# Kernel tuning notes

Measured on AMD Instinct MI355X. Metric: run time of the kernel, lower is better.

Reference implementation:

```python
import jax, jax.numpy as jnp
import numpy as np

S = 2048   # sample_batch
N = 16     # num_h (agents per sample group)
OBS = 8
PRED = 12
H = 16     # hidden / embed size


def _lstm_cell(x, h, c, Wi, Wh, b):
    # torch LSTMCell gate order: i, f, g, o
    g = x @ Wi + h @ Wh + b
    i, f, gg, o = jnp.split(g, 4, axis=-1)
    c = jax.nn.sigmoid(f) * c + jax.nn.sigmoid(i) * jnp.tanh(gg)
    h = jax.nn.sigmoid(o) * jnp.tanh(c)
    return h, c


def setup_inputs() -> dict:
    key = jax.random.key(0)
    ks = jax.random.split(key, 16)
    B = S * N
    p = lambda k, sh: jax.random.normal(k, sh, jnp.float32) * 0.1
    return dict(
        traj_rel=jax.random.normal(ks[0], (OBS, B, 2), jnp.float32),
        obs_traj_pos=jax.random.normal(ks[1], (OBS, B, 2), jnp.float32),
        nei_index=jax.random.randint(ks[2], (B, N), 0, 2, jnp.int32),
        noise=jax.random.normal(ks[3], (PRED, B, 2), jnp.float32),
        enc_emb_W=p(ks[4], (2, H)), enc_emb_b=jnp.zeros((H,), jnp.float32),
        enc_Wi=p(ks[5], (H, 4 * H)), enc_Wh=p(ks[6], (H, 4 * H)), enc_b=jnp.zeros((4 * H,), jnp.float32),
        dec_in_W=p(ks[7], (H + 2, H)), dec_in_b=jnp.zeros((H,), jnp.float32),
        dec_Wi=p(ks[8], (H, 4 * H)), dec_Wh=p(ks[9], (H, 4 * H)), dec_b=jnp.zeros((4 * H,), jnp.float32),
        pool_rel_W=p(ks[10], (2, H)), pool_rel_b=jnp.zeros((H,), jnp.float32),
        pool_mlp_W=p(ks[11], (2 * H, H)), pool_mlp_b=jnp.zeros((H,), jnp.float32),
        out_W=p(ks[12], (H, 4)), out_b=jnp.zeros((4,), jnp.float32),
    )


def reference(traj_rel, obs_traj_pos, nei_index, noise,
              enc_emb_W, enc_emb_b, enc_Wi, enc_Wh, enc_b,
              dec_in_W, dec_in_b, dec_Wi, dec_Wh, dec_b,
              pool_rel_W, pool_rel_b, pool_mlp_W, pool_mlp_b,
              out_W, out_b):
    B = traj_rel.shape[1]
    mask = nei_index > 0  # (B, N)

    # --- history encoder: embed + LSTM over obs steps, take last hidden ---
    def enc_step(carry, x):
        h, c = carry
        e = jax.nn.relu(x @ enc_emb_W + enc_emb_b)
        h, c = _lstm_cell(e, h, c, enc_Wi, enc_Wh, enc_b)
        return (h, c), None

    h0 = jnp.zeros((B, H), traj_rel.dtype)
    (h_enc, _), _ = jax.lax.scan(enc_step, (h0, h0), traj_rel[:OBS])

    # --- neighbor pooling: embed relative pos, concat neighbor hidden, MLP, masked max-pool ---
    def pool(rel, h):
        re = jax.nn.relu(rel @ pool_rel_W + pool_rel_b)  # (B, N, H)
        hn = jnp.broadcast_to(h.reshape(S, 1, N, H), (S, N, N, H)).reshape(B, N, H)
        feat = jax.nn.relu(jnp.concatenate([re, hn], -1) @ pool_mlp_W + pool_mlp_b)
        masked = jnp.where(mask[..., None], feat, -1e9)
        pooled = masked.max(axis=1)  # (B, H)
        has = mask.any(axis=1, keepdims=True)
        return jnp.where(has, pooled, 0.0)

    def dec_step(carry, noise_t):
        h, c, ctx, out, pos = carry
        inp = jax.lax.stop_gradient(jnp.concatenate([ctx, out], -1))  # .detach() in torch
        e = jax.nn.relu(inp @ dec_in_W + dec_in_b)
        h, c = _lstm_cell(e, h, c, dec_Wi, dec_Wh, dec_b)
        p = pos.reshape(S, N, 2)
        # rel[s,i,j] = pos[s,i] - pos[s,j]  (matches expand/transpose subtraction)
        rel = (p[:, :, None, :] - p[:, None, :, :]).reshape(B, N, 2)
        ctx = pool(rel, h)
        o4 = (h + ctx) @ out_W + out_b
        mu = o4[:, :2]
        scale = jnp.clip(o4[:, 2:], -9.0, 4.0)
        std = jnp.exp(scale)
        pred = mu + std * noise_t
        pos = jax.lax.stop_gradient(pos + pred)
        return (h, c, ctx, pred, pos), (pred, mu, std)

    init = (h_enc, jnp.zeros_like(h_enc), jnp.zeros_like(h_enc),
            traj_rel[OBS - 1], obs_traj_pos[-1])
    _, (pred, mu, std) = jax.lax.scan(dec_step, init, noise)
    return pred, mu, std  # each (PRED, B, 2)
```

## Files before the change

kernel.cpp:

```cpp
#include <hip/hip_runtime.h>

#define S_    2048
#define N_    16
#define OBS_  8
#define PRED_ 12
#define B_    (S_*N_)

typedef __attribute__((ext_vector_type(8))) short short8;
typedef __attribute__((ext_vector_type(4))) float floatx4;
typedef __attribute__((ext_vector_type(4))) unsigned uintx4;
typedef unsigned short ushort_t;

__device__ __forceinline__ float sigmf(float x) { return __builtin_amdgcn_rcpf(1.0f + __expf(-x)); }
__device__ __forceinline__ float tanhx(float x) { return fmaf(-2.0f, __builtin_amdgcn_rcpf(1.0f + __expf(2.0f*x)), 1.0f); }
__device__ __forceinline__ unsigned bfhi(float f) {
  return __builtin_bit_cast(unsigned, f) + 0x8000u;
}
__device__ __forceinline__ unsigned pack2bf(float lo, float hi) {
  return __builtin_amdgcn_perm(bfhi(hi), bfhi(lo), 0x07060302);
}
__device__ __forceinline__ ushort_t f2bf1(float f) { return (ushort_t)(bfhi(f) >> 16); }

extern "C" __global__ __launch_bounds__(256, 4) void traj_ar_kernel(
    const float* __restrict__ traj_rel, const float* __restrict__ obs_pos,
    const int*  __restrict__ nei,       const float* __restrict__ noise,
    const float* __restrict__ eeW, const float* __restrict__ eeb,
    const float* __restrict__ eWi, const float* __restrict__ eWh, const float* __restrict__ eb,
    const float* __restrict__ diW, const float* __restrict__ dib,
    const float* __restrict__ dWi, const float* __restrict__ dWh, const float* __restrict__ db,
    const float* __restrict__ prW, const float* __restrict__ prb,
    const float* __restrict__ mW,  const float* __restrict__ mb,
    const float* __restrict__ oW,  const float* __restrict__ ob,
    float* __restrict__ out)
{
  __shared__ __align__(16) float sW_pr[32];
  __shared__ __align__(16) float sb_pr[16];
  __shared__ __align__(16) float sW_o[64];
  __shared__ __align__(16) float sb_o[4];
  __shared__ __align__(16) float h_s[256];
  __shared__ __align__(16) float ctx_s[256];
  __shared__ __align__(16) float g_s[4*256];
  __shared__ __align__(16) ushort_t e_bf[16*24];
  __shared__ __align__(16) ushort_t hb_s[16*24];
  __shared__ __align__(16) ushort_t ctx_bf[16*24];
  __shared__ __align__(16) ushort_t re_s[16*392];
  __shared__ __align__(16) float pos_s[32];
  __shared__ __align__(16) float prev_s[32];
  __shared__ __align__(16) ushort_t prev_bf[32];
  __shared__            unsigned sm_s[16];

  const int tid = threadIdx.x;
  const int s = blockIdx.x;
  const int i = tid >> 4;
  const int k = tid & 15;
  const int bi = s*N_ + i;
  const int lq = (tid & 63) >> 4;
  const int lc = tid & 15;
  const int w  = tid >> 6;

  if (tid < 32) sW_pr[tid] = prW[tid];
  if (tid < 16) sb_pr[tid] = prb[tid];
  if (tid < 64) sW_o[tid] = oW[tid];
  if (tid < 4)  sb_o[tid] = ob[tid];
  if (tid < 192) ((unsigned*)hb_s)[tid] = 0;
  if (tid < 192) ((unsigned*)ctx_bf)[tid] = 0;

  if (k < 2) {
    float pv = traj_rel[((OBS_-1)*B_ + bi)*2 + k];
    prev_s[i*2+k] = pv;
    prev_bf[i*2+k] = f2bf1(pv);
    pos_s[i*2+k]  = obs_pos[((OBS_-1)*B_ + bi)*2 + k];
  }

  short8 bfrag;
  {
    uintx4 bw;
    #pragma unroll
    for (int p = 0; p < 4; ++p)
      bw[p] = pack2bf(mW[(8*lq + 2*p)*16 + lc], mW[(8*lq + 2*p + 1)*16 + lc]);
    bfrag = __builtin_bit_cast(short8, bw);
  }
  const float bm = mb[lc];

  const float w0k = eeW[k], w1k = eeW[16+k], bek = eeb[k];

  short8 gA; floatx4 gC;
  {
    const int row0 = (lq & 1) * 8;
    const float* gsrc = (lq & 2) ? eWh : eWi;
    uintx4 aw;
    #pragma unroll
    for (int p = 0; p < 4; ++p)
      aw[p] = pack2bf(gsrc[(row0+2*p)*64 + w*16 + lc], gsrc[(row0+2*p+1)*64 + w*16 + lc]);
    gA = __builtin_bit_cast(short8, aw);
    #pragma unroll
    for (int r = 0; r < 4; ++r) gC[r] = eb[w*16 + lq*4 + r];
  }

  unsigned long long bal = __ballot(nei[bi*N_ + k] > 0);
  if (k == 0) sm_s[i] = (unsigned)((bal >> (16*(i & 3))) & 0xFFFFull);

  __syncthreads();

  float c_reg = 0.0f;
  const float2* xr2 = (const float2*)traj_rel;
  for (int t = 0; t < OBS_; ++t) {
    {
      float2 x = xr2[t*B_ + bi];
      float e = fmaxf(fmaf(x.y, w1k, fmaf(x.x, w0k, bek)), 0.0f);
      e_bf[i*24 + k] = f2bf1(e);
    }
    __syncthreads();
    {
      const ushort_t* bp = (lq < 2) ? &e_bf[lc*24 + (lq&1)*8] : &hb_s[lc*24 + (lq&1)*8];
      short8 bfr = *(const short8*)bp;
      floatx4 d = __builtin_amdgcn_mfma_f32_16x16x32_bf16(gA, bfr, gC, 0, 0, 0);
      *(floatx4*)&g_s[w*256 + lc*16 + lq*4] = d;
    }
    __syncthreads();
    {
      float gI = g_s[0*256 + i*16 + k];
      float gF = g_s[1*256 + i*16 + k];
      float gG = g_s[2*256 + i*16 + k];
      float gO = g_s[3*256 + i*16 + k];
      float ig = sigmf(gI), fg = sigmf(gF), gv = tanhx(gG), og = sigmf(gO);
      c_reg = fg*c_reg + ig*gv;
      float nh = og * tanhx(c_reg);
      hb_s[i*24 + k] = f2bf1(nh);
    }
  }

  short8 dA; floatx4 dC;
  {
    const int row0 = (lq & 1) * 8;
    const float* gsrc = (lq & 2) ? dWh : dWi;
    uintx4 aw;
    #pragma unroll
    for (int p = 0; p < 4; ++p)
      aw[p] = pack2bf(gsrc[(row0+2*p)*64 + w*16 + lc], gsrc[(row0+2*p+1)*64 + w*16 + lc]);
    dA = __builtin_bit_cast(short8, aw);
    #pragma unroll
    for (int r = 0; r < 4; ++r) dC[r] = db[w*16 + lq*4 + r];
  }

  short8 diA; floatx4 diC;
  {
    uintx4 aw; aw[0]=0; aw[1]=0; aw[2]=0; aw[3]=0;
    if (lq < 2) {
      const int r0 = lq*8;
      #pragma unroll
      for (int p = 0; p < 4; ++p)
        aw[p] = pack2bf(diW[(r0+2*p)*16 + lc], diW[(r0+2*p+1)*16 + lc]);
    } else if (lq == 2) {
      aw[0] = pack2bf(diW[16*16 + lc], diW[17*16 + lc]);
    }
    diA = __builtin_bit_cast(short8, aw);
    #pragma unroll
    for (int r = 0; r < 4; ++r) diC[r] = dib[lq*4 + r];
  }

  floatx4 cm0, cm1, cm2, cm3;
  {
    #pragma unroll
    for (int tt = 0; tt < 4; ++tt) {
      const unsigned mi = sm_s[4*w + tt];
      floatx4 cf;
      #pragma unroll
      for (int r = 0; r < 4; ++r)
        cf[r] = ((mi >> (lq*4 + r)) & 1u) ? bm : -1e9f;
      if (tt==0) cm0=cf; else if (tt==1) cm1=cf; else if (tt==2) cm2=cf; else cm3=cf;
    }
  }

  c_reg = 0.0f;
  const int MU_OFF = PRED_*B_*2;
  const int SD_OFF = 2*PRED_*B_*2;
  for (int t = 0; t < PRED_; ++t) {
    const float nz = noise[(t*B_ + bi)*2 + (k & 1)];
    {
      short8 cv = *(const short8*)&ctx_bf[lc*24 + (lq&1)*8];
      uintx4 pz; pz[0] = *(const unsigned*)&prev_bf[lc*2]; pz[1]=0; pz[2]=0; pz[3]=0;
      short8 pv = __builtin_bit_cast(short8, pz);
      short8 zz = {0,0,0,0,0,0,0,0};
      short8 bfr = (lq < 2) ? cv : ((lq == 2) ? pv : zz);
      floatx4 d = __builtin_amdgcn_mfma_f32_16x16x32_bf16(diA, bfr, diC, 0, 0, 0);
      if (w == 0) {
        uint2 ep;
        ep.x = pack2bf(fmaxf(d[0],0.0f), fmaxf(d[1],0.0f));
        ep.y = pack2bf(fmaxf(d[2],0.0f), fmaxf(d[3],0.0f));
        *(uint2*)&e_bf[lc*24 + lq*4] = ep;
      }
    }
    __syncthreads();
    {
      const ushort_t* bp = (lq < 2) ? &e_bf[lc*24 + (lq&1)*8] : &hb_s[lc*24 + (lq&1)*8];
      short8 bfr = *(const short8*)bp;
      floatx4 d = __builtin_amdgcn_mfma_f32_16x16x32_bf16(dA, bfr, dC, 0, 0, 0);
      *(floatx4*)&g_s[w*256 + lc*16 + lq*4] = d;
    }
    __syncthreads();
    {
      float gI = g_s[0*256 + i*16 + k];
      float gF = g_s[1*256 + i*16 + k];
      float gG = g_s[2*256 + i*16 + k];
      float gO = g_s[3*256 + i*16 + k];
      float ig = sigmf(gI), fg = sigmf(gF), gv = tanhx(gG), og = sigmf(gO);
      c_reg = fg*c_reg + ig*gv;
      float nh = og * tanhx(c_reg);
      h_s[i*16 + k] = nh;
      hb_s[i*24 + k] = f2bf1(nh);
    }
    {
      float rx = pos_s[i*2+0] - pos_s[k*2+0];
      float ry = pos_s[i*2+1] - pos_s[k*2+1];
      uintx4 v0, v1;
      #pragma unroll
      for (int m = 0; m < 4; ++m) {
        float a0 = fmaxf(fmaf(ry, sW_pr[16+2*m], fmaf(rx, sW_pr[2*m],   sb_pr[2*m])),   0.0f);
        float a1 = fmaxf(fmaf(ry, sW_pr[17+2*m], fmaf(rx, sW_pr[2*m+1], sb_pr[2*m+1])), 0.0f);
        float b0 = fmaxf(fmaf(ry, sW_pr[24+2*m], fmaf(rx, sW_pr[8+2*m], sb_pr[8+2*m])), 0.0f);
        float b1 = fmaxf(fmaf(ry, sW_pr[25+2*m], fmaf(rx, sW_pr[9+2*m], sb_pr[9+2*m])), 0.0f);
        v0[m] = pack2bf(a0, a1);
        v1[m] = pack2bf(b0, b1);
      }
      uintx4* rp = (uintx4*)&re_s[i*392 + k*24];
      rp[0] = v0;
      rp[1] = v1;
    }
    __syncthreads();
    {
      const ushort_t* hbp = &hb_s[lc*24 + (lq-2)*8];
      #pragma unroll
      for (int tt = 0; tt < 4; ++tt) {
        const int it = 4*w + tt;
        const ushort_t* rep = &re_s[it*392 + lc*24 + lq*8];
        const ushort_t* ap = (lq < 2) ? rep : hbp;
        short8 a = *(const short8*)ap;
        const floatx4 cm = (tt==0)?cm0:(tt==1)?cm1:(tt==2)?cm2:cm3;
        floatx4 d = __builtin_amdgcn_mfma_f32_16x16x32_bf16(a, bfrag, cm, 0, 0, 0);
        float pm = fmaxf(fmaxf(d[0], d[1]), fmaxf(d[2], d[3]));
        pm = fmaxf(pm, __shfl_xor(pm, 16, 64));
        pm = fmaxf(pm, __shfl_xor(pm, 32, 64));
        if (lq == tt) {
          float cv = fmaxf(pm, 0.0f);
          ctx_s[it*16 + lc] = cv;
          ctx_bf[it*24 + lc] = f2bf1(cv);
        }
      }
    }
    {
      float o4v = 0.0f;
      if (k < 4) {
        const float* hp = &h_s[i*16];
        const float* cx = &ctx_s[i*16];
        float acc = sb_o[k];
        #pragma unroll
        for (int m = 0; m < 16; ++m) acc = fmaf(hp[m]+cx[m], sW_o[m*4+k], acc);
        o4v = acc;
      }
      float sc = __shfl_down(o4v, 2, 64);
      if (k < 2) {
        float mu = o4v;
        float scale = fminf(fmaxf(sc, -9.0f), 4.0f);
        float sd = __expf(scale);
        float pr = fmaf(sd, nz, mu);
        int o = (t*B_ + bi)*2 + k;
        out[o]          = pr;
        out[MU_OFF + o] = mu;
        out[SD_OFF + o] = sd;
        pos_s[i*2+k] += pr;
        prev_s[i*2+k] = pr;
        prev_bf[i*2+k] = f2bf1(pr);
      }
    }
    __syncthreads();
  }
  (void)prev_s;
}

extern "C" void kernel_launch(void* const* d_in, const int* in_sizes, int n_in,
                              void* d_out, int out_size, void* d_ws, size_t ws_size,
                              hipStream_t stream) {
  (void)in_sizes; (void)n_in; (void)d_ws; (void)ws_size; (void)out_size;
  traj_ar_kernel<<<dim3(S_), dim3(256), 0, stream>>>(
      (const float*)d_in[0],  (const float*)d_in[1],  (const int*)d_in[2],   (const float*)d_in[3],
      (const float*)d_in[4],  (const float*)d_in[5],  (const float*)d_in[6], (const float*)d_in[7],
      (const float*)d_in[8],  (const float*)d_in[9],  (const float*)d_in[10],(const float*)d_in[11],
      (const float*)d_in[12], (const float*)d_in[13], (const float*)d_in[14],(const float*)d_in[15],
      (const float*)d_in[16], (const float*)d_in[17], (const float*)d_in[18],(const float*)d_in[19],
      (float*)d_out);
}
```

Measured before the change: 174.5 us.

## Replicate LSTM gate MFMAs per wave to drop cross-wave gate exchange barriers

Each wave now computes all four LSTM gates itself with four MFMAs and keeps them in registers, instead of each wave computing one gate and swapping results through shared memory. Embedding and hidden buffers become per-wave private copies, and context, position and previous-output buffers are double-buffered. Together this cuts the block barriers to zero per encoder step and one per decoder step. The cost is four times the gate MFMA and activation work per wave, plus more registers for the gate fragments.

```diff
diff --git a/kernel.cpp b/kernel.cpp
--- a/kernel.cpp
+++ b/kernel.cpp
@@ -39,14 +39,12 @@
   __shared__ __align__(16) float sb_o[4];
   __shared__ __align__(16) float h_s[256];
   __shared__ __align__(16) float ctx_s[256];
-  __shared__ __align__(16) float g_s[4*256];
-  __shared__ __align__(16) ushort_t e_bf[16*24];
-  __shared__ __align__(16) ushort_t hb_s[16*24];
-  __shared__ __align__(16) ushort_t ctx_bf[16*24];
+  __shared__ __align__(16) ushort_t e_w[4*384];
+  __shared__ __align__(16) ushort_t h_w[4*384];
+  __shared__ __align__(16) ushort_t ctx_bf[2][384];
+  __shared__ __align__(16) float pos_s[2][32];
+  __shared__ __align__(16) ushort_t prev_bf[2][32];
   __shared__ __align__(16) ushort_t re_s[16*392];
-  __shared__ __align__(16) float pos_s[32];
-  __shared__ __align__(16) float prev_s[32];
-  __shared__ __align__(16) ushort_t prev_bf[32];
   __shared__            unsigned sm_s[16];
 
   const int tid = threadIdx.x;
@@ -57,19 +55,23 @@
   const int lq = (tid & 63) >> 4;
   const int lc = tid & 15;
   const int w  = tid >> 6;
+  const int l  = tid & 63;
+  const int u0 = lq*4;
 
   if (tid < 32) sW_pr[tid] = prW[tid];
   if (tid < 16) sb_pr[tid] = prb[tid];
   if (tid < 64) sW_o[tid] = oW[tid];
   if (tid < 4)  sb_o[tid] = ob[tid];
-  if (tid < 192) ((unsigned*)hb_s)[tid] = 0;
   if (tid < 192) ((unsigned*)ctx_bf)[tid] = 0;
+  {
+    unsigned* hz = (unsigned*)&h_w[w*384];
+    hz[l] = 0; hz[64+l] = 0; hz[128+l] = 0;
+  }
 
   if (k < 2) {
     float pv = traj_rel[((OBS_-1)*B_ + bi)*2 + k];
-    prev_s[i*2+k] = pv;
-    prev_bf[i*2+k] = f2bf1(pv);
-    pos_s[i*2+k]  = obs_pos[((OBS_-1)*B_ + bi)*2 + k];
+    prev_bf[0][i*2+k] = f2bf1(pv);
+    pos_s[0][i*2+k]  = obs_pos[((OBS_-1)*B_ + bi)*2 + k];
   }
 
   short8 bfrag;
@@ -82,66 +84,73 @@
   }
   const float bm = mb[lc];
 
-  const float w0k = eeW[k], w1k = eeW[16+k], bek = eeb[k];
-
-  short8 gA; floatx4 gC;
-  {
-    const int row0 = (lq & 1) * 8;
-    const float* gsrc = (lq & 2) ? eWh : eWi;
-    uintx4 aw;
-    #pragma unroll
-    for (int p = 0; p < 4; ++p)
-      aw[p] = pack2bf(gsrc[(row0+2*p)*64 + w*16 + lc], gsrc[(row0+2*p+1)*64 + w*16 + lc]);
-    gA = __builtin_bit_cast(short8, aw);
-    #pragma unroll
-    for (int r = 0; r < 4; ++r) gC[r] = eb[w*16 + lq*4 + r];
-  }
+  float ew0[4], ew1[4], ebv[4];
+  #pragma unroll
+  for (int r = 0; r < 4; ++r) {
+    ew0[r] = eeW[u0+r]; ew1[r] = eeW[16+u0+r]; ebv[r] = eeb[u0+r];
+  }
+
+  const int row0 = (lq & 1) * 8;
+
+  #define LOAD_GATE_FRAG(A, C, Wi_, Wh_, bias_, g) {                                   \
+    const float* gsrc_ = (lq & 2) ? (Wh_) : (Wi_);                                     \
+    uintx4 aw_;                                                                        \
+    aw_[0] = pack2bf(gsrc_[(row0+0)*64 + (g)*16 + lc], gsrc_[(row0+1)*64 + (g)*16 + lc]); \
+    aw_[1] = pack2bf(gsrc_[(row0+2)*64 + (g)*16 + lc], gsrc_[(row0+3)*64 + (g)*16 + lc]); \
+    aw_[2] = pack2bf(gsrc_[(row0+4)*64 + (g)*16 + lc], gsrc_[(row0+5)*64 + (g)*16 + lc]); \
+    aw_[3] = pack2bf(gsrc_[(row0+6)*64 + (g)*16 + lc], gsrc_[(row0+7)*64 + (g)*16 + lc]); \
+    (A) = __builtin_bit_cast(short8, aw_);                                             \
+    (C)[0] = (bias_)[(g)*16 + u0 + 0]; (C)[1] = (bias_)[(g)*16 + u0 + 1];              \
+    (C)[2] = (bias_)[(g)*16 + u0 + 2]; (C)[3] = (bias_)[(g)*16 + u0 + 3];              \
+  }
+
+  short8 eA0, eA1, eA2, eA3; floatx4 eC0, eC1, eC2, eC3;
+  LOAD_GATE_FRAG(eA0, eC0, eWi, eWh, eb, 0);
+  LOAD_GATE_FRAG(eA1, eC1, eWi, eWh, eb, 1);
+  LOAD_GATE_FRAG(eA2, eC2, eWi, eWh, eb, 2);
+  LOAD_GATE_FRAG(eA3, eC3, eWi, eWh, eb, 3);
 
   unsigned long long bal = __ballot(nei[bi*N_ + k] > 0);
   if (k == 0) sm_s[i] = (unsigned)((bal >> (16*(i & 3))) & 0xFFFFull);
 
   __syncthreads();
 
-  float c_reg = 0.0f;
+  ushort_t* ewp = &e_w[w*384];
+  ushort_t* hwp = &h_w[w*384];
+
+  #define LSTM_EW(r, hv) {                                                            \
+    float ig = sigmf(dI[r]), fg = sigmf(dF[r]), gv = tanhx(dG[r]), og = sigmf(dO[r]); \
+    c4[r] = fg*c4[r] + ig*gv;                                                         \
+    hv = og * tanhx(c4[r]);                                                           \
+  }
+
+  floatx4 c4 = {0.0f, 0.0f, 0.0f, 0.0f};
   const float2* xr2 = (const float2*)traj_rel;
   for (int t = 0; t < OBS_; ++t) {
-    {
-      float2 x = xr2[t*B_ + bi];
-      float e = fmaxf(fmaf(x.y, w1k, fmaf(x.x, w0k, bek)), 0.0f);
-      e_bf[i*24 + k] = f2bf1(e);
-    }
-    __syncthreads();
-    {
-      const ushort_t* bp = (lq < 2) ? &e_bf[lc*24 + (lq&1)*8] : &hb_s[lc*24 + (lq&1)*8];
-      short8 bfr = *(const short8*)bp;
-      floatx4 d = __builtin_amdgcn_mfma_f32_16x16x32_bf16(gA, bfr, gC, 0, 0, 0);
-      *(floatx4*)&g_s[w*256 + lc*16 + lq*4] = d;
-    }
-    __syncthreads();
-    {
-      float gI = g_s[0*256 + i*16 + k];
-      float gF = g_s[1*256 + i*16 + k];
-      float gG = g_s[2*256 + i*16 + k];
-      float gO = g_s[3*256 + i*16 + k];
-      float ig = sigmf(gI), fg = sigmf(gF), gv = tanhx(gG), og = sigmf(gO);
-      c_reg = fg*c_reg + ig*gv;
-      float nh = og * tanhx(c_reg);
-      hb_s[i*24 + k] = f2bf1(nh);
-    }
-  }
-
-  short8 dA; floatx4 dC;
-  {
-    const int row0 = (lq & 1) * 8;
-    const float* gsrc = (lq & 2) ? dWh : dWi;
-    uintx4 aw;
-    #pragma unroll
-    for (int p = 0; p < 4; ++p)
-      aw[p] = pack2bf(gsrc[(row0+2*p)*64 + w*16 + lc], gsrc[(row0+2*p+1)*64 + w*16 + lc]);
-    dA = __builtin_bit_cast(short8, aw);
-    #pragma unroll
-    for (int r = 0; r < 4; ++r) dC[r] = db[w*16 + lq*4 + r];
-  }
+    float2 x = xr2[t*B_ + s*N_ + lc];
+    float e0 = fmaxf(fmaf(x.y, ew1[0], fmaf(x.x, ew0[0], ebv[0])), 0.0f);
+    float e1 = fmaxf(fmaf(x.y, ew1[1], fmaf(x.x, ew0[1], ebv[1])), 0.0f);
+    float e2 = fmaxf(fmaf(x.y, ew1[2], fmaf(x.x, ew0[2], ebv[2])), 0.0f);
+    float e3 = fmaxf(fmaf(x.y, ew1[3], fmaf(x.x, ew0[3], ebv[3])), 0.0f);
+    uint2 ep; ep.x = pack2bf(e0, e1); ep.y = pack2bf(e2, e3);
+    *(uint2*)&ewp[lc*24 + u0] = ep;
+    const ushort_t* bp = (lq < 2) ? &ewp[lc*24 + (lq&1)*8] : &hwp[lc*24 + (lq&1)*8];
+    short8 bfr = *(const short8*)bp;
+    floatx4 dI = __builtin_amdgcn_mfma_f32_16x16x32_bf16(eA0, bfr, eC0, 0, 0, 0);
+    floatx4 dF = __builtin_amdgcn_mfma_f32_16x16x32_bf16(eA1, bfr, eC1, 0, 0, 0);
+    floatx4 dG = __builtin_amdgcn_mfma_f32_16x16x32_bf16(eA2, bfr, eC2, 0, 0, 0);
+    floatx4 dO = __builtin_amdgcn_mfma_f32_16x16x32_bf16(eA3, bfr, eC3, 0, 0, 0);
+    float h40, h41, h42, h43;
+    LSTM_EW(0, h40); LSTM_EW(1, h41); LSTM_EW(2, h42); LSTM_EW(3, h43);
+    uint2 hp2; hp2.x = pack2bf(h40, h41); hp2.y = pack2bf(h42, h43);
+    *(uint2*)&hwp[lc*24 + u0] = hp2;
+  }
+
+  short8 dA0, dA1, dA2, dA3; floatx4 dC0, dC1, dC2, dC3;
+  LOAD_GATE_FRAG(dA0, dC0, dWi, dWh, db, 0);
+  LOAD_GATE_FRAG(dA1, dC1, dWi, dWh, db, 1);
+  LOAD_GATE_FRAG(dA2, dC2, dWi, dWh, db, 2);
+  LOAD_GATE_FRAG(dA3, dC3, dWi, dWh, db, 3);
 
   short8 diA; floatx4 diC;
   {
@@ -156,7 +165,7 @@
     }
     diA = __builtin_bit_cast(short8, aw);
     #pragma unroll
-    for (int r = 0; r < 4; ++r) diC[r] = dib[lq*4 + r];
+    for (int r = 0; r < 4; ++r) diC[r] = dib[u0 + r];
   }
 
   floatx4 cm0, cm1, cm2, cm3;
@@ -172,47 +181,43 @@
     }
   }
 
-  c_reg = 0.0f;
+  c4 = (floatx4){0.0f, 0.0f, 0.0f, 0.0f};
   const int MU_OFF = PRED_*B_*2;
   const int SD_OFF = 2*PRED_*B_*2;
   for (int t = 0; t < PRED_; ++t) {
+    const int p = t & 1;
     const float nz = noise[(t*B_ + bi)*2 + (k & 1)];
     {
-      short8 cv = *(const short8*)&ctx_bf[lc*24 + (lq&1)*8];
-      uintx4 pz; pz[0] = *(const unsigned*)&prev_bf[lc*2]; pz[1]=0; pz[2]=0; pz[3]=0;
+      short8 cv = *(const short8*)&ctx_bf[p][lc*24 + (lq&1)*8];
+      uintx4 pz; pz[0] = *(const unsigned*)&prev_bf[p][lc*2]; pz[1]=0; pz[2]=0; pz[3]=0;
       short8 pv = __builtin_bit_cast(short8, pz);
       short8 zz = {0,0,0,0,0,0,0,0};
-      short8 bfr = (lq < 2) ? cv : ((lq == 2) ? pv : zz);
-      floatx4 d = __builtin_amdgcn_mfma_f32_16x16x32_bf16(diA, bfr, diC, 0, 0, 0);
-      if (w == 0) {
-        uint2 ep;
-        ep.x = pack2bf(fmaxf(d[0],0.0f), fmaxf(d[1],0.0f));
-        ep.y = pack2bf(fmaxf(d[2],0.0f), fmaxf(d[3],0.0f));
-        *(uint2*)&e_bf[lc*24 + lq*4] = ep;
-      }
-    }
-    __syncthreads();
-    {
-      const ushort_t* bp = (lq < 2) ? &e_bf[lc*24 + (lq&1)*8] : &hb_s[lc*24 + (lq&1)*8];
+      short8 bf1 = (lq < 2) ? cv : ((lq == 2) ? pv : zz);
+      floatx4 d = __builtin_amdgcn_mfma_f32_16x16x32_bf16(diA, bf1, diC, 0, 0, 0);
+      uint2 ep;
+      ep.x = pack2bf(fmaxf(d[0],0.0f), fmaxf(d[1],0.0f));
+      ep.y = pack2bf(fmaxf(d[2],0.0f), fmaxf(d[3],0.0f));
+      *(uint2*)&ewp[lc*24 + u0] = ep;
+    }
+    {
+      const ushort_t* bp = (lq < 2) ? &ewp[lc*24 + (lq&1)*8] : &hwp[lc*24 + (lq&1)*8];
       short8 bfr = *(const short8*)bp;
-      floatx4 d = __builtin_amdgcn_mfma_f32_16x16x32_bf16(dA, bfr, dC, 0, 0, 0);
-      *(floatx4*)&g_s[w*256 + lc*16 + lq*4] = d;
-    }
-    __syncthreads();
-    {
-      float gI = g_s[0*256 + i*16 + k];
-      float gF = g_s[1*256 + i*16 + k];
-      float gG = g_s[2*256 + i*16 + k];
-      float gO = g_s[3*256 + i*16 + k];
-      float ig = sigmf(gI), fg = sigmf(gF), gv = tanhx(gG), og = sigmf(gO);
-      c_reg = fg*c_reg + ig*gv;
-      float nh = og * tanhx(c_reg);
-      h_s[i*16 + k] = nh;
-      hb_s[i*24 + k] = f2bf1(nh);
-    }
-    {
-      float rx = pos_s[i*2+0] - pos_s[k*2+0];
-      float ry = pos_s[i*2+1] - pos_s[k*2+1];
+      floatx4 dI = __builtin_amdgcn_mfma_f32_16x16x32_bf16(dA0, bfr, dC0, 0, 0, 0);
+      floatx4 dF = __builtin_amdgcn_mfma_f32_16x16x32_bf16(dA1, bfr, dC1, 0, 0, 0);
+      floatx4 dG = __builtin_amdgcn_mfma_f32_16x16x32_bf16(dA2, bfr, dC2, 0, 0, 0);
+      floatx4 dO = __builtin_amdgcn_mfma_f32_16x16x32_bf16(dA3, bfr, dC3, 0, 0, 0);
+      float h40, h41, h42, h43;
+      LSTM_EW(0, h40); LSTM_EW(1, h41); LSTM_EW(2, h42); LSTM_EW(3, h43);
+      uint2 hp2; hp2.x = pack2bf(h40, h41); hp2.y = pack2bf(h42, h43);
+      *(uint2*)&hwp[lc*24 + u0] = hp2;
+      if ((lc >> 2) == w) {
+        floatx4 hv; hv[0]=h40; hv[1]=h41; hv[2]=h42; hv[3]=h43;
+        *(floatx4*)&h_s[lc*16 + u0] = hv;
+      }
+    }
+    {
+      float rx = pos_s[p][i*2+0] - pos_s[p][k*2+0];
+      float ry = pos_s[p][i*2+1] - pos_s[p][k*2+1];
       uintx4 v0, v1;
       #pragma unroll
       for (int m = 0; m < 4; ++m) {
@@ -227,24 +232,23 @@
       rp[0] = v0;
       rp[1] = v1;
     }
-    __syncthreads();
-    {
-      const ushort_t* hbp = &hb_s[lc*24 + (lq-2)*8];
+    {
+      const ushort_t* hbp = &hwp[lc*24 + (lq-2)*8];
       #pragma unroll
       for (int tt = 0; tt < 4; ++tt) {
         const int it = 4*w + tt;
         const ushort_t* rep = &re_s[it*392 + lc*24 + lq*8];
         const ushort_t* ap = (lq < 2) ? rep : hbp;
         short8 a = *(const short8*)ap;
-        const floatx4 cm = (tt==0)?cm0:(tt==1)?cm1:(tt==2)?cm2:cm3;
-        floatx4 d = __builtin_amdgcn_mfma_f32_16x16x32_bf16(a, bfrag, cm, 0, 0, 0);
+        const floatx4 cmv = (tt==0)?cm0:(tt==1)?cm1:(tt==2)?cm2:cm3;
+        floatx4 d = __builtin_amdgcn_mfma_f32_16x16x32_bf16(a, bfrag, cmv, 0, 0, 0);
         float pm = fmaxf(fmaxf(d[0], d[1]), fmaxf(d[2], d[3]));
         pm = fmaxf(pm, __shfl_xor(pm, 16, 64));
         pm = fmaxf(pm, __shfl_xor(pm, 32, 64));
         if (lq == tt) {
-          float cv = fmaxf(pm, 0.0f);
-          ctx_s[it*16 + lc] = cv;
-          ctx_bf[it*24 + lc] = f2bf1(cv);
+          float cvv = fmaxf(pm, 0.0f);
+          ctx_s[it*16 + lc] = cvv;
+          ctx_bf[p^1][it*24 + lc] = f2bf1(cvv);
         }
       }
     }
@@ -268,14 +272,14 @@
         out[o]          = pr;
         out[MU_OFF + o] = mu;
         out[SD_OFF + o] = sd;
-        pos_s[i*2+k] += pr;
-        prev_s[i*2+k] = pr;
-        prev_bf[i*2+k] = f2bf1(pr);
+        pos_s[p^1][i*2+k] = pos_s[p][i*2+k] + pr;
+        prev_bf[p^1][i*2+k] = f2bf1(pr);
       }
     }
     __syncthreads();
   }
-  (void)prev_s;
+  #undef LSTM_EW
+  #undef LOAD_GATE_FRAG
 }
 
 extern "C" void kernel_launch(void* const* d_in, const int* in_sizes, int n_in,
```

New measurement: 202.8 us. 16.2% more time.
